# Kernel tuning notes

Hardware: AMD Instinct MI355X
Metric: run time of the kernel (lower is better)

## Reference

```python
import jax, jax.numpy as jnp
import numpy as np
from math import sqrt

IN_DIM = 4096
OUT_DIM = 32
TW = 2            # tree_width (forced to 2 by the forward's pairwise stacking)
TREE_DEPTH = 22
T = TREE_DEPTH - 1  # number of loop iterations (module decrements tree_depth)


def _w(k, out_dim, in_dim):
    # mimics init_weights_unif: U(-1,1)/sqrt(out_dim) + eye (preserve=True default)
    x = (jax.random.uniform(k, (out_dim, in_dim)) * 2 - 1) / sqrt(out_dim)
    return x + jnp.eye(out_dim, in_dim)


def _b(k, dim):
    return (jax.random.uniform(k, (dim,)) * 2 - 1) / sqrt(dim)


def setup_inputs() -> dict:
    key = jax.random.key(0)
    ks = jax.random.split(key, 14)
    return {
        "x": jax.random.normal(ks[0], (IN_DIM,), dtype=jnp.float32),
        "in_left_layer": _w(ks[1], TW, IN_DIM),
        "in_right_layer": _w(ks[2], TW, IN_DIM),
        "in_left_bias": _b(ks[3], TW),
        "in_right_bias": _b(ks[4], TW),
        "tree_left_layers": jnp.stack([_w(k, TW, TW) for k in jax.random.split(ks[5], T)]),
        "tree_right_layers": jnp.stack([_w(k, TW, TW) for k in jax.random.split(ks[6], T)]),
        "tree_left_biases": jnp.stack([_b(k, TW) for k in jax.random.split(ks[7], T)]),
        "tree_right_biases": jnp.stack([_b(k, TW) for k in jax.random.split(ks[8], T)]),
        "out_layer0": _w(ks[9], OUT_DIM, IN_DIM),
        "out_layers": jnp.stack([_w(k, OUT_DIM, TW) for k in jax.random.split(ks[10], T)]),
        "out_bias": _b(ks[11], OUT_DIM),
    }


def reference(x, in_left_layer, in_right_layer, in_left_bias, in_right_bias,
              tree_left_layers, tree_right_layers, tree_left_biases,
              tree_right_biases, out_layer0, out_layers, out_bias):
    # Faithful to BinTreeNetwork.forward: the per-j torch.tensor([li_j, ri_j])
    # construction is exactly jnp.stack([left, right], axis=1); the
    # ComponentNetwork is constructed in __init__ but never used in forward.
    left = x @ in_left_layer.T + in_left_bias      # (TW,)
    right = x @ in_right_layer.T + in_right_bias   # (TW,)
    out = x @ out_layer0.T                          # (OUT_DIM,)
    n_iter = tree_left_layers.shape[0]
    for i in range(n_iter):  # fixed small structural loop; shapes differ per level
        # res: binary-tree expansion, shape (2,)*(i+2); res[j,0]=left[j], res[j,1]=right[j]
        res = jnp.stack([left, right], axis=1)
        left = res @ tree_left_layers[i].T + tree_left_biases[i]
        right = res @ tree_right_layers[i].T + tree_right_biases[i]
        # out broadcasts: (2,)*i+(OUT_DIM,) + (2,)*(i+1)+(OUT_DIM,)
        out = out + res @ out_layers[i].T
    return out + out_bias  # shape (2,)*T + (OUT_DIM,)
```

## Files before the change

### kernel.cpp

```cpp
#include <hip/hip_runtime.h>
#include <hip/hip_bf16.h>


#define P0 (1u << 19)
#define C14OFF (1u << 20)

typedef float floatx4 __attribute__((ext_vector_type(4)));

__global__ __launch_bounds__(1024) void k_prefix(
    const float* __restrict__ x,
    const float* __restrict__ inL,
    const float* __restrict__ inR,
    const float* __restrict__ inLb,
    const float* __restrict__ inRb,
    const float* __restrict__ treeL,
    const float* __restrict__ treeR,
    const float* __restrict__ treeLb,
    const float* __restrict__ treeRb,
    const float* __restrict__ outL0,
    const float* __restrict__ outLs,
    const float* __restrict__ outB,
    float* __restrict__ ws)
{
    __shared__ float xs[4096];
    __shared__ float dots[36];
    const int tid = threadIdx.x;

    if (tid < 1024)
        ((floatx4*)xs)[tid] = ((const floatx4*)x)[tid];
    __syncthreads();

    const int wave = tid >> 6, lane = tid & 63;
    for (int d = wave; d < 36; d += 16) {
        const float* row =
            (d < 2) ? inL + d * 4096 :
            (d < 4) ? inR + (d - 2) * 4096 :
                      outL0 + (d - 4) * 4096;
        const floatx4* r4 = (const floatx4*)row;
        const floatx4* x4 = (const floatx4*)xs;
        float s = 0.f;
        for (int k = lane; k < 1024; k += 64) {
            floatx4 a = r4[k], b = x4[k];
            s += a.x * b.x + a.y * b.y + a.z * b.z + a.w * b.w;
        }
        #pragma unroll
        for (int off = 32; off; off >>= 1) s += __shfl_down(s, off, 64);
        if (lane == 0) dots[d] = s;
    }
    __syncthreads();

    float* base  = ws + P0;
    float* outLf = ws + P0 + 32;
    float* tLf   = ws + P0 + 1376;
    float* tRf   = ws + P0 + 1460;
    float* tLbf  = ws + P0 + 1544;
    float* tRbf  = ws + P0 + 1586;
    float* C7    = ws + P0 + 2048;

    for (int i = tid; i < 21 * 64; i += 1024) outLf[i] = outLs[i];
    if (tid < 84)                      tLf[tid]        = treeL[tid];
    else if (tid < 168)                tRf[tid - 84]   = treeR[tid - 84];
    else if (tid < 210)                tLbf[tid - 168] = treeLb[tid - 168];
    else if (tid < 252)                tRbf[tid - 210] = treeRb[tid - 210];
    if (tid < 32) base[tid] = dots[4 + tid] + outB[tid];
    if (tid < 2) {
        ws[tid * 2 + 0] = dots[tid]     + inLb[tid];
        ws[tid * 2 + 1] = dots[2 + tid] + inRb[tid];
    }
    __syncthreads();

    for (int i = 1; i <= 13; ++i) {
        const float* prev = ws + ((1u << (i + 1)) - 4);
        float* cur        = ws + ((1u << (i + 2)) - 4);
        const int rows = 1 << (i + 1);
        const int lowmask = (1 << (i - 1)) - 1;
        for (int m = tid; m < rows; m += 1024) {
            const int src = ((m >> i) << (i - 1)) | (m & lowmask);
            const int s = (m >> (i - 1)) & 1;
            const float* W  = (s ? tRf  : tLf)  + (i - 1) * 4;
            const float* bb = (s ? tRbf : tLbf) + (i - 1) * 2;
            const float p0 = prev[src * 2], p1 = prev[src * 2 + 1];
            cur[m * 2 + 0] = W[0] * p0 + W[1] * p1 + bb[0];
            cur[m * 2 + 1] = W[2] * p0 + W[3] * p1 + bb[1];
        }
        __syncthreads();
    }

    for (int idx = tid; idx < 8192; idx += 1024) {
        const int m = idx >> 5, o = idx & 31;
        float s = base[o];
        #pragma unroll
        for (int i = 0; i < 8; ++i) {
            const float* ri = ws + ((1u << (i + 2)) - 4) + (m & ((2 << i) - 1)) * 2;
            s += ri[0] * outLf[i * 64 + o * 2] + ri[1] * outLf[i * 64 + o * 2 + 1];
        }
        C7[idx] = s;
    }
}

__global__ __launch_bounds__(256) void k_mid(float* __restrict__ ws)
{
    const int blk = blockIdx.x;
    int j, b;
    if      (blk < 16) { j = 14; b = blk; }
    else if (blk < 48) { j = 15; b = blk - 16; }
    else               { j = 16; b = blk - 48; }

    const float* tLf  = ws + P0 + 1376;
    const float* tRf  = ws + P0 + 1460;
    const float* tLbf = ws + P0 + 1544;
    const float* tRbf = ws + P0 + 1586;

    unsigned m = (unsigned)b << 11;
    const unsigned basej = m;
    unsigned sbits = 0;
    for (int l = j; l > 13; --l) {
        sbits |= ((m >> (l - 1)) & 1u) << l;
        m = ((m >> l) << (l - 1)) | (m & ((1u << (l - 1)) - 1));
    }

    const int r0 = threadIdx.x * 8;
    const floatx4* s4 = (const floatx4*)(ws + ((1u << 15) - 4) + (m + r0) * 2);
    floatx4 a0 = s4[0], a1 = s4[1], a2 = s4[2], a3 = s4[3];
    float r[8][2] = {{a0.x,a0.y},{a0.z,a0.w},{a1.x,a1.y},{a1.z,a1.w},
                     {a2.x,a2.y},{a2.z,a2.w},{a3.x,a3.y},{a3.z,a3.w}};

    for (int l = 14; l <= j; ++l) {
        const int s = (sbits >> l) & 1;
        const float* W  = (s ? tRf  : tLf)  + (l - 1) * 4;
        const float* bb = (s ? tRbf : tLbf) + (l - 1) * 2;
        const float w00 = W[0], w01 = W[1], w10 = W[2], w11 = W[3];
        const float b0 = bb[0], b1 = bb[1];
        #pragma unroll
        for (int q = 0; q < 8; ++q) {
            const float p0 = r[q][0], p1 = r[q][1];
            r[q][0] = w00 * p0 + w01 * p1 + b0;
            r[q][1] = w10 * p0 + w11 * p1 + b1;
        }
    }

    floatx4* d4 = (floatx4*)(ws + ((1u << (j + 2)) - 4) + (basej + r0) * 2);
    d4[0] = (floatx4){r[0][0], r[0][1], r[1][0], r[1][1]};
    d4[1] = (floatx4){r[2][0], r[2][1], r[3][0], r[3][1]};
    d4[2] = (floatx4){r[4][0], r[4][1], r[5][0], r[5][1]};
    d4[3] = (floatx4){r[6][0], r[6][1], r[7][0], r[7][1]};
}

__global__ __launch_bounds__(256) void k_c14(float* __restrict__ ws)
{
    const unsigned m = blockIdx.x * 256u + threadIdx.x;
    const float* outLf = ws + P0 + 32;
    const float* C7    = ws + P0 + 2048;

    float acc[32];
    const floatx4* c4 = (const floatx4*)(C7 + (m & 255u) * 32);
    #pragma unroll
    for (int q = 0; q < 8; ++q) {
        floatx4 v = c4[q];
        acc[q * 4 + 0] = v.x; acc[q * 4 + 1] = v.y;
        acc[q * 4 + 2] = v.z; acc[q * 4 + 3] = v.w;
    }
    #pragma unroll
    for (int i = 8; i <= 14; ++i) {
        const float2 v = *(const float2*)(ws + ((1u << (i + 2)) - 4)
                                             + (m & ((2u << i) - 1)) * 2);
        const float* cf = outLf + i * 64;
        #pragma unroll
        for (int o = 0; o < 32; ++o)
            acc[o] += v.x * cf[o * 2] + v.y * cf[o * 2 + 1];
    }
    floatx4* dst = (floatx4*)(ws + C14OFF + m * 32);
    #pragma unroll
    for (int q = 0; q < 8; ++q)
        dst[q] = (floatx4){acc[q * 4 + 0], acc[q * 4 + 1],
                           acc[q * 4 + 2], acc[q * 4 + 3]};
}

__global__ __launch_bounds__(256) void k_final_fold(const float* __restrict__ ws,
                                                    float* __restrict__ out)
{
    __shared__ floatx4 st[256 * 8];
    const int tid = threadIdx.x;
    const unsigned B = blockIdx.x * 256u + tid;
    const float* outLf = ws + P0 + 32;
    const float* tLf   = ws + P0 + 1376;
    const float* tRf   = ws + P0 + 1460;
    const float* tLbf  = ws + P0 + 1544;
    const float* tRbf  = ws + P0 + 1586;
    const float* C14   = ws + C14OFF;

    float acc[32];
    {
        const floatx4* c4 = (const floatx4*)(C14 + (B & 0x7FFFu) * 32);
        #pragma unroll
        for (int q = 0; q < 8; ++q) {
            floatx4 v = c4[q];
            acc[q * 4 + 0] = v.x; acc[q * 4 + 1] = v.y;
            acc[q * 4 + 2] = v.z; acc[q * 4 + 3] = v.w;
        }
    }

    {
        const float2 v = *(const float2*)(ws + ((1u << 17) - 4)
                                             + (B & 0xFFFFu) * 2);
        const float* cf = outLf + 15 * 64;
        #pragma unroll
        for (int o = 0; o < 32; ++o)
            acc[o] += v.x * cf[o * 2] + v.y * cf[o * 2 + 1];
    }

    {
        const unsigned Blo = B & 0xFFFFu;
        const float* r16 = ws + ((1u << 18) - 4);
        const float2* rA = (const float2*)(r16 + Blo * 2);
        const float2* rC = (const float2*)(r16 + (Blo + 65536u) * 2);
        float2 vA = *rA, vC = *rC;
        float A0 = vA.x, A1 = vA.y;
        float c0 = vC.x, c1 = vC.y;
        {
            const int pick = (B >> 16) & 1;
            const float q0 = pick ? c0 : A0, q1 = pick ? c1 : A1;
            const float* cf = outLf + 16 * 64;
            #pragma unroll
            for (int o = 0; o < 32; ++o)
                acc[o] += q0 * cf[o * 2] + q1 * cf[o * 2 + 1];
        }
        #pragma unroll
        for (int l = 17; l <= 20; ++l) {
            const int s = (B >> (l - 1)) & 1;
            const float* WL = tLf + (l - 1) * 4;
            const float* WR = tRf + (l - 1) * 4;
            const float* bL = tLbf + (l - 1) * 2;
            const float* bR = tRbf + (l - 1) * 2;
            const float w00 = s ? WR[0] : WL[0], w01 = s ? WR[1] : WL[1];
            const float w10 = s ? WR[2] : WL[2], w11 = s ? WR[3] : WL[3];
            const float b0  = s ? bR[0] : bL[0], b1  = s ? bR[1] : bL[1];
            const float nA0 = w00 * A0 + w01 * A1 + b0;
            const float nA1 = w10 * A0 + w11 * A1 + b1;
            const float nc0 = w00 * c0 + w01 * c1 + b0;
            const float nc1 = w10 * c0 + w11 * c1 + b1;
            A0 = nA0; A1 = nA1; c0 = nc0; c1 = nc1;
            const int pick = (B >> l) & 1;
            const float q0 = pick ? c0 : A0, q1 = pick ? c1 : A1;
            const float* cf = outLf + l * 64;
            #pragma unroll
            for (int o = 0; o < 32; ++o)
                acc[o] += q0 * cf[o * 2] + q1 * cf[o * 2 + 1];
        }
    }

    #pragma unroll
    for (int q = 0; q < 8; ++q) {
        st[tid * 8 + (q ^ (tid & 7))] =
            (floatx4){acc[q * 4 + 0], acc[q * 4 + 1],
                      acc[q * 4 + 2], acc[q * 4 + 3]};
    }
    __syncthreads();
    {
        const int w = tid >> 6, lane = tid & 63;
        const int x = (lane & 7) ^ (lane >> 3);
        floatx4* dst = (floatx4*)(out + (size_t)blockIdx.x * 8192u
                                      + (unsigned)w * 2048u + (unsigned)lane * 4u);
        #pragma unroll
        for (int j = 0; j < 8; ++j) {
            const int m = w * 64 + j * 8 + (lane >> 3);
            __builtin_nontemporal_store(st[m * 8 + x], dst + j * 64);
        }
    }
}

__global__ __launch_bounds__(256) void k_final_legacy(const float* __restrict__ ws,
                                                      float* __restrict__ out)
{
    __shared__ floatx4 st[256 * 8];
    const int tid = threadIdx.x;
    const unsigned B = blockIdx.x * 256u + tid;
    const float* outLf = ws + P0 + 32;
    const float* tLf   = ws + P0 + 1376;
    const float* tRf   = ws + P0 + 1460;
    const float* tLbf  = ws + P0 + 1544;
    const float* tRbf  = ws + P0 + 1586;
    const float* C7    = ws + P0 + 2048;

    float acc[32];
    {
        const floatx4* c4 = (const floatx4*)(C7 + (B & 255u) * 32);
        #pragma unroll
        for (int q = 0; q < 8; ++q) {
            floatx4 v = c4[q];
            acc[q * 4 + 0] = v.x; acc[q * 4 + 1] = v.y;
            acc[q * 4 + 2] = v.z; acc[q * 4 + 3] = v.w;
        }
    }
    float p[8][2];
    #pragma unroll
    for (int i = 8; i <= 15; ++i) {
        const float2* ri = (const float2*)(ws + ((1u << (i + 2)) - 4)
                                              + (B & ((2u << i) - 1)) * 2);
        float2 v = *ri;
        p[i - 8][0] = v.x;
        p[i - 8][1] = v.y;
    }
    #pragma unroll
    for (int i = 0; i < 8; ++i) {
        const float* cf = outLf + (i + 8) * 64;
        const float q0 = p[i][0], q1 = p[i][1];
        #pragma unroll
        for (int o = 0; o < 32; ++o)
            acc[o] += q0 * cf[o * 2] + q1 * cf[o * 2 + 1];
    }
    {
        const unsigned Blo = B & 0xFFFFu;
        const float* r16 = ws + ((1u << 18) - 4);
        const float2* rA = (const float2*)(r16 + Blo * 2);
        const float2* rC = (const float2*)(r16 + (Blo + 65536u) * 2);
        float2 vA = *rA, vC = *rC;
        float A0 = vA.x, A1 = vA.y;
        float c0 = vC.x, c1 = vC.y;
        {
            const int pick = (B >> 16) & 1;
            const float q0 = pick ? c0 : A0, q1 = pick ? c1 : A1;
            const float* cf = outLf + 16 * 64;
            #pragma unroll
            for (int o = 0; o < 32; ++o)
                acc[o] += q0 * cf[o * 2] + q1 * cf[o * 2 + 1];
        }
        #pragma unroll
        for (int l = 17; l <= 20; ++l) {
            const int s = (B >> (l - 1)) & 1;
            const float* WL = tLf + (l - 1) * 4;
            const float* WR = tRf + (l - 1) * 4;
            const float* bL = tLbf + (l - 1) * 2;
            const float* bR = tRbf + (l - 1) * 2;
            const float w00 = s ? WR[0] : WL[0], w01 = s ? WR[1] : WL[1];
            const float w10 = s ? WR[2] : WL[2], w11 = s ? WR[3] : WL[3];
            const float b0  = s ? bR[0] : bL[0], b1  = s ? bR[1] : bL[1];
            const float nA0 = w00 * A0 + w01 * A1 + b0;
            const float nA1 = w10 * A0 + w11 * A1 + b1;
            const float nc0 = w00 * c0 + w01 * c1 + b0;
            const float nc1 = w10 * c0 + w11 * c1 + b1;
            A0 = nA0; A1 = nA1; c0 = nc0; c1 = nc1;
            const int pick = (B >> l) & 1;
            const float q0 = pick ? c0 : A0, q1 = pick ? c1 : A1;
            const float* cf = outLf + l * 64;
            #pragma unroll
            for (int o = 0; o < 32; ++o)
                acc[o] += q0 * cf[o * 2] + q1 * cf[o * 2 + 1];
        }
    }
    #pragma unroll
    for (int q = 0; q < 8; ++q) {
        st[tid * 8 + (q ^ (tid & 7))] =
            (floatx4){acc[q * 4 + 0], acc[q * 4 + 1],
                      acc[q * 4 + 2], acc[q * 4 + 3]};
    }
    __syncthreads();
    {
        const int w = tid >> 6, lane = tid & 63;
        const int x = (lane & 7) ^ (lane >> 3);
        floatx4* dst = (floatx4*)(out + (size_t)blockIdx.x * 8192u
                                      + (unsigned)w * 2048u + (unsigned)lane * 4u);
        #pragma unroll
        for (int j = 0; j < 8; ++j) {
            const int m = w * 64 + j * 8 + (lane >> 3);
            __builtin_nontemporal_store(st[m * 8 + x], dst + j * 64);
        }
    }
}

extern "C" void kernel_launch(void* const* d_in, const int* in_sizes, int n_in,
                              void* d_out, int out_size, void* d_ws, size_t ws_size,
                              hipStream_t stream) {
    const float* x     = (const float*)d_in[0];
    const float* inL   = (const float*)d_in[1];
    const float* inR   = (const float*)d_in[2];
    const float* inLb  = (const float*)d_in[3];
    const float* inRb  = (const float*)d_in[4];
    const float* treeL = (const float*)d_in[5];
    const float* treeR = (const float*)d_in[6];
    const float* treeLb= (const float*)d_in[7];
    const float* treeRb= (const float*)d_in[8];
    const float* outL0 = (const float*)d_in[9];
    const float* outLs = (const float*)d_in[10];
    const float* outB  = (const float*)d_in[11];
    float* ws = (float*)d_ws;
    float* out = (float*)d_out;

    const bool use_fold = ws_size >= ((size_t)C14OFF + (1u << 20)) * sizeof(float);

    hipLaunchKernelGGL(k_prefix, dim3(1), dim3(1024), 0, stream,
                       x, inL, inR, inLb, inRb, treeL, treeR, treeLb, treeRb,
                       outL0, outLs, outB, ws);
    hipLaunchKernelGGL(k_mid, dim3(112), dim3(256), 0, stream, ws);
    if (use_fold) {
        hipLaunchKernelGGL(k_c14, dim3(128), dim3(256), 0, stream, ws);
        hipLaunchKernelGGL(k_final_fold, dim3(1u << 13), dim3(256), 0, stream, ws, out);
    } else {
        hipLaunchKernelGGL(k_final_legacy, dim3(1u << 13), dim3(256), 0, stream, ws, out);
    }
}
```

Before: 379.7 us.

## Split dot products across blocks and precompute prefix sums through level sixteen

Measured after the change: 360.4 us. 1.05x faster.

```diff
diff --git a/kernel.cpp b/kernel.cpp
--- a/kernel.cpp
+++ b/kernel.cpp
@@ -4,57 +4,58 @@
 
 #define P0 (1u << 19)
 #define C14OFF (1u << 20)
+#define C16OFF (1u << 21)
 
 typedef float floatx4 __attribute__((ext_vector_type(4)));
 
-__global__ __launch_bounds__(1024) void k_prefix(
+__global__ __launch_bounds__(1024) void k_dots(
     const float* __restrict__ x,
     const float* __restrict__ inL,
     const float* __restrict__ inR,
+    const float* __restrict__ outL0,
+    float* __restrict__ ws)
+{
+    __shared__ float red[16];
+    const int d = blockIdx.x;
+    const int tid = threadIdx.x;
+    const float* row =
+        (d < 2) ? inL + d * 4096 :
+        (d < 4) ? inR + (d - 2) * 4096 :
+                  outL0 + (d - 4) * 4096;
+    floatx4 a = ((const floatx4*)row)[tid];
+    floatx4 b = ((const floatx4*)x)[tid];
+    float s = a.x * b.x + a.y * b.y + a.z * b.z + a.w * b.w;
+    #pragma unroll
+    for (int off = 32; off; off >>= 1) s += __shfl_down(s, off, 64);
+    if ((tid & 63) == 0) red[tid >> 6] = s;
+    __syncthreads();
+    if (tid < 16) {
+        float v = red[tid];
+        #pragma unroll
+        for (int off = 8; off; off >>= 1) v += __shfl_down(v, off, 16);
+        if (tid == 0) ws[P0 + 1664 + d] = v;
+    }
+}
+
+__global__ __launch_bounds__(1024) void k_levels(
     const float* __restrict__ inLb,
     const float* __restrict__ inRb,
     const float* __restrict__ treeL,
     const float* __restrict__ treeR,
     const float* __restrict__ treeLb,
     const float* __restrict__ treeRb,
-    const float* __restrict__ outL0,
     const float* __restrict__ outLs,
     const float* __restrict__ outB,
     float* __restrict__ ws)
 {
-    __shared__ float xs[4096];
-    __shared__ float dots[36];
     const int tid = threadIdx.x;
-
-    if (tid < 1024)
-        ((floatx4*)xs)[tid] = ((const floatx4*)x)[tid];
-    __syncthreads();
-
-    const int wave = tid >> 6, lane = tid & 63;
-    for (int d = wave; d < 36; d += 16) {
-        const float* row =
-            (d < 2) ? inL + d * 4096 :
-            (d < 4) ? inR + (d - 2) * 4096 :
-                      outL0 + (d - 4) * 4096;
-        const floatx4* r4 = (const floatx4*)row;
-        const floatx4* x4 = (const floatx4*)xs;
-        float s = 0.f;
-        for (int k = lane; k < 1024; k += 64) {
-            floatx4 a = r4[k], b = x4[k];
-            s += a.x * b.x + a.y * b.y + a.z * b.z + a.w * b.w;
-        }
-        #pragma unroll
-        for (int off = 32; off; off >>= 1) s += __shfl_down(s, off, 64);
-        if (lane == 0) dots[d] = s;
-    }
-    __syncthreads();
-
     float* base  = ws + P0;
     float* outLf = ws + P0 + 32;
     float* tLf   = ws + P0 + 1376;
     float* tRf   = ws + P0 + 1460;
     float* tLbf  = ws + P0 + 1544;
     float* tRbf  = ws + P0 + 1586;
+    const float* dots = ws + P0 + 1664;
     float* C7    = ws + P0 + 2048;
 
     for (int i = tid; i < 21 * 64; i += 1024) outLf[i] = outLs[i];
@@ -146,7 +147,7 @@
     d4[3] = (floatx4){r[6][0], r[6][1], r[7][0], r[7][1]};
 }
 
-__global__ __launch_bounds__(256) void k_c14(float* __restrict__ ws)
+__global__ __launch_bounds__(256) void k_c16(float* __restrict__ ws)
 {
     const unsigned m = blockIdx.x * 256u + threadIdx.x;
     const float* outLf = ws + P0 + 32;
@@ -161,6 +162,36 @@
         acc[q * 4 + 2] = v.z; acc[q * 4 + 3] = v.w;
     }
     #pragma unroll
+    for (int i = 8; i <= 16; ++i) {
+        const float2 v = *(const float2*)(ws + ((1u << (i + 2)) - 4)
+                                             + (m & ((2u << i) - 1)) * 2);
+        const float* cf = outLf + i * 64;
+        #pragma unroll
+        for (int o = 0; o < 32; ++o)
+            acc[o] += v.x * cf[o * 2] + v.y * cf[o * 2 + 1];
+    }
+    floatx4* dst = (floatx4*)(ws + C16OFF + (size_t)m * 32);
+    #pragma unroll
+    for (int q = 0; q < 8; ++q)
+        dst[q] = (floatx4){acc[q * 4 + 0], acc[q * 4 + 1],
+                           acc[q * 4 + 2], acc[q * 4 + 3]};
+}
+
+__global__ __launch_bounds__(256) void k_c14(float* __restrict__ ws)
+{
+    const unsigned m = blockIdx.x * 256u + threadIdx.x;
+    const float* outLf = ws + P0 + 32;
+    const float* C7    = ws + P0 + 2048;
+
+    float acc[32];
+    const floatx4* c4 = (const floatx4*)(C7 + (m & 255u) * 32);
+    #pragma unroll
+    for (int q = 0; q < 8; ++q) {
+        floatx4 v = c4[q];
+        acc[q * 4 + 0] = v.x; acc[q * 4 + 1] = v.y;
+        acc[q * 4 + 2] = v.z; acc[q * 4 + 3] = v.w;
+    }
+    #pragma unroll
     for (int i = 8; i <= 14; ++i) {
         const float2 v = *(const float2*)(ws + ((1u << (i + 2)) - 4)
                                              + (m & ((2u << i) - 1)) * 2);
@@ -176,8 +207,8 @@
                            acc[q * 4 + 2], acc[q * 4 + 3]};
 }
 
-__global__ __launch_bounds__(256) void k_final_fold(const float* __restrict__ ws,
-                                                    float* __restrict__ out)
+__global__ __launch_bounds__(256) void k_final_c16(const float* __restrict__ ws,
+                                                   float* __restrict__ out)
 {
     __shared__ floatx4 st[256 * 8];
     const int tid = threadIdx.x;
@@ -187,11 +218,11 @@
     const float* tRf   = ws + P0 + 1460;
     const float* tLbf  = ws + P0 + 1544;
     const float* tRbf  = ws + P0 + 1586;
-    const float* C14   = ws + C14OFF;
+    const float* C16   = ws + C16OFF;
 
     float acc[32];
     {
-        const floatx4* c4 = (const floatx4*)(C14 + (B & 0x7FFFu) * 32);
+        const floatx4* c4 = (const floatx4*)(C16 + (size_t)(B & 0x1FFFFu) * 32);
         #pragma unroll
         for (int q = 0; q < 8; ++q) {
             floatx4 v = c4[q];
@@ -201,30 +232,12 @@
     }
 
     {
-        const float2 v = *(const float2*)(ws + ((1u << 17) - 4)
-                                             + (B & 0xFFFFu) * 2);
-        const float* cf = outLf + 15 * 64;
-        #pragma unroll
-        for (int o = 0; o < 32; ++o)
-            acc[o] += v.x * cf[o * 2] + v.y * cf[o * 2 + 1];
-    }
-
-    {
         const unsigned Blo = B & 0xFFFFu;
         const float* r16 = ws + ((1u << 18) - 4);
-        const float2* rA = (const float2*)(r16 + Blo * 2);
-        const float2* rC = (const float2*)(r16 + (Blo + 65536u) * 2);
-        float2 vA = *rA, vC = *rC;
+        float2 vA = *(const float2*)(r16 + Blo * 2);
+        float2 vC = *(const float2*)(r16 + (Blo + 65536u) * 2);
         float A0 = vA.x, A1 = vA.y;
         float c0 = vC.x, c1 = vC.y;
-        {
-            const int pick = (B >> 16) & 1;
-            const float q0 = pick ? c0 : A0, q1 = pick ? c1 : A1;
-            const float* cf = outLf + 16 * 64;
-            #pragma unroll
-            for (int o = 0; o < 32; ++o)
-                acc[o] += q0 * cf[o * 2] + q1 * cf[o * 2 + 1];
-        }
         #pragma unroll
         for (int l = 17; l <= 20; ++l) {
             const int s = (B >> (l - 1)) & 1;
@@ -269,8 +282,8 @@
     }
 }
 
-__global__ __launch_bounds__(256) void k_final_legacy(const float* __restrict__ ws,
-                                                      float* __restrict__ out)
+__global__ __launch_bounds__(256) void k_final_fold(const float* __restrict__ ws,
+                                                    float* __restrict__ out)
 {
     __shared__ floatx4 st[256 * 8];
     const int tid = threadIdx.x;
@@ -280,11 +293,11 @@
     const float* tRf   = ws + P0 + 1460;
     const float* tLbf  = ws + P0 + 1544;
     const float* tRbf  = ws + P0 + 1586;
-    const float* C7    = ws + P0 + 2048;
+    const float* C14   = ws + C14OFF;
 
     float acc[32];
     {
-        const floatx4* c4 = (const floatx4*)(C7 + (B & 255u) * 32);
+        const floatx4* c4 = (const floatx4*)(C14 + (B & 0x7FFFu) * 32);
         #pragma unroll
         for (int q = 0; q < 8; ++q) {
             floatx4 v = c4[q];
@@ -292,29 +305,19 @@
             acc[q * 4 + 2] = v.z; acc[q * 4 + 3] = v.w;
         }
     }
-    float p[8][2];
-    #pragma unroll
-    for (int i = 8; i <= 15; ++i) {
-        const float2* ri = (const float2*)(ws + ((1u << (i + 2)) - 4)
-                                              + (B & ((2u << i) - 1)) * 2);
-        float2 v = *ri;
-        p[i - 8][0] = v.x;
-        p[i - 8][1] = v.y;
-    }
-    #pragma unroll
-    for (int i = 0; i < 8; ++i) {
-        const float* cf = outLf + (i + 8) * 64;
-        const float q0 = p[i][0], q1 = p[i][1];
+    {
+        const float2 v = *(const float2*)(ws + ((1u << 17) - 4)
+                                             + (B & 0xFFFFu) * 2);
+        const float* cf = outLf + 15 * 64;
         #pragma unroll
         for (int o = 0; o < 32; ++o)
-            acc[o] += q0 * cf[o * 2] + q1 * cf[o * 2 + 1];
+            acc[o] += v.x * cf[o * 2] + v.y * cf[o * 2 + 1];
     }
     {
         const unsigned Blo = B & 0xFFFFu;
         const float* r16 = ws + ((1u << 18) - 4);
-        const float2* rA = (const float2*)(r16 + Blo * 2);
-        const float2* rC = (const float2*)(r16 + (Blo + 65536u) * 2);
-        float2 vA = *rA, vC = *rC;
+        float2 vA = *(const float2*)(r16 + Blo * 2);
+        float2 vC = *(const float2*)(r16 + (Blo + 65536u) * 2);
         float A0 = vA.x, A1 = vA.y;
         float c0 = vC.x, c1 = vC.y;
         {
@@ -368,6 +371,104 @@
     }
 }
 
+__global__ __launch_bounds__(256) void k_final_legacy(const float* __restrict__ ws,
+                                                      float* __restrict__ out)
+{
+    __shared__ floatx4 st[256 * 8];
+    const int tid = threadIdx.x;
+    const unsigned B = blockIdx.x * 256u + tid;
+    const float* outLf = ws + P0 + 32;
+    const float* tLf   = ws + P0 + 1376;
+    const float* tRf   = ws + P0 + 1460;
+    const float* tLbf  = ws + P0 + 1544;
+    const float* tRbf  = ws + P0 + 1586;
+    const float* C7    = ws + P0 + 2048;
+
+    float acc[32];
+    {
+        const floatx4* c4 = (const floatx4*)(C7 + (B & 255u) * 32);
+        #pragma unroll
+        for (int q = 0; q < 8; ++q) {
+            floatx4 v = c4[q];
+            acc[q * 4 + 0] = v.x; acc[q * 4 + 1] = v.y;
+            acc[q * 4 + 2] = v.z; acc[q * 4 + 3] = v.w;
+        }
+    }
+    float p[8][2];
+    #pragma unroll
+    for (int i = 8; i <= 15; ++i) {
+        const float2* ri = (const float2*)(ws + ((1u << (i + 2)) - 4)
+                                              + (B & ((2u << i) - 1)) * 2);
+        float2 v = *ri;
+        p[i - 8][0] = v.x;
+        p[i - 8][1] = v.y;
+    }
+    #pragma unroll
+    for (int i = 0; i < 8; ++i) {
+        const float* cf = outLf + (i + 8) * 64;
+        const float q0 = p[i][0], q1 = p[i][1];
+        #pragma unroll
+        for (int o = 0; o < 32; ++o)
+            acc[o] += q0 * cf[o * 2] + q1 * cf[o * 2 + 1];
+    }
+    {
+        const unsigned Blo = B & 0xFFFFu;
+        const float* r16 = ws + ((1u << 18) - 4);
+        float2 vA = *(const float2*)(r16 + Blo * 2);
+        float2 vC = *(const float2*)(r16 + (Blo + 65536u) * 2);
+        float A0 = vA.x, A1 = vA.y;
+        float c0 = vC.x, c1 = vC.y;
+        {
+            const int pick = (B >> 16) & 1;
+            const float q0 = pick ? c0 : A0, q1 = pick ? c1 : A1;
+            const float* cf = outLf + 16 * 64;
+            #pragma unroll
+            for (int o = 0; o < 32; ++o)
+                acc[o] += q0 * cf[o * 2] + q1 * cf[o * 2 + 1];
+        }
+        #pragma unroll
+        for (int l = 17; l <= 20; ++l) {
+            const int s = (B >> (l - 1)) & 1;
+            const float* WL = tLf + (l - 1) * 4;
+            const float* WR = tRf + (l - 1) * 4;
+            const float* bL = tLbf + (l - 1) * 2;
+            const float* bR = tRbf + (l - 1) * 2;
+            const float w00 = s ? WR[0] : WL[0], w01 = s ? WR[1] : WL[1];
+            const float w10 = s ? WR[2] : WL[2], w11 = s ? WR[3] : WL[3];
+            const float b0  = s ? bR[0] : bL[0], b1  = s ? bR[1] : bL[1];
+            const float nA0 = w00 * A0 + w01 * A1 + b0;
+            const float nA1 = w10 * A0 + w11 * A1 + b1;
+            const float nc0 = w00 * c0 + w01 * c1 + b0;
+            const float nc1 = w10 * c0 + w11 * c1 + b1;
+            A0 = nA0; A1 = nA1; c0 = nc0; c1 = nc1;
+            const int pick = (B >> l) & 1;
+            const float q0 = pick ? c0 : A0, q1 = pick ? c1 : A1;
+            const float* cf = outLf + l * 64;
+            #pragma unroll
+            for (int o = 0; o < 32; ++o)
+                acc[o] += q0 * cf[o * 2] + q1 * cf[o * 2 + 1];
+        }
+    }
+    #pragma unroll
+    for (int q = 0; q < 8; ++q) {
+        st[tid * 8 + (q ^ (tid & 7))] =
+            (floatx4){acc[q * 4 + 0], acc[q * 4 + 1],
+                      acc[q * 4 + 2], acc[q * 4 + 3]};
+    }
+    __syncthreads();
+    {
+        const int w = tid >> 6, lane = tid & 63;
+        const int x = (lane & 7) ^ (lane >> 3);
+        floatx4* dst = (floatx4*)(out + (size_t)blockIdx.x * 8192u
+                                      + (unsigned)w * 2048u + (unsigned)lane * 4u);
+        #pragma unroll
+        for (int j = 0; j < 8; ++j) {
+            const int m = w * 64 + j * 8 + (lane >> 3);
+            __builtin_nontemporal_store(st[m * 8 + x], dst + j * 64);
+        }
+    }
+}
+
 extern "C" void kernel_launch(void* const* d_in, const int* in_sizes, int n_in,
                               void* d_out, int out_size, void* d_ws, size_t ws_size,
                               hipStream_t stream) {
@@ -386,13 +487,18 @@
     float* ws = (float*)d_ws;
     float* out = (float*)d_out;
 
-    const bool use_fold = ws_size >= ((size_t)C14OFF + (1u << 20)) * sizeof(float);
-
-    hipLaunchKernelGGL(k_prefix, dim3(1), dim3(1024), 0, stream,
-                       x, inL, inR, inLb, inRb, treeL, treeR, treeLb, treeRb,
-                       outL0, outLs, outB, ws);
+    const bool use_c16 = ws_size >= ((size_t)C16OFF + (1u << 22)) * sizeof(float);
+    const bool use_c14 = ws_size >= ((size_t)C14OFF + (1u << 20)) * sizeof(float);
+
+    hipLaunchKernelGGL(k_dots, dim3(36), dim3(1024), 0, stream,
+                       x, inL, inR, outL0, ws);
+    hipLaunchKernelGGL(k_levels, dim3(1), dim3(1024), 0, stream,
+                       inLb, inRb, treeL, treeR, treeLb, treeRb, outLs, outB, ws);
     hipLaunchKernelGGL(k_mid, dim3(112), dim3(256), 0, stream, ws);
-    if (use_fold) {
+    if (use_c16) {
+        hipLaunchKernelGGL(k_c16, dim3(512), dim3(256), 0, stream, ws);
+        hipLaunchKernelGGL(k_final_c16, dim3(1u << 13), dim3(256), 0, stream, ws, out);
+    } else if (use_c14) {
         hipLaunchKernelGGL(k_c14, dim3(128), dim3(256), 0, stream, ws);
         hipLaunchKernelGGL(k_final_fold, dim3(1u << 13), dim3(256), 0, stream, ws, out);
     } else {
```
